# Kernel tuning notes

Hardware: AMD Instinct MI355X
Metric: run time of the kernel (lower is better)

Reference implementation:

```python
import jax, jax.numpy as jnp
import numpy as np


def _causal_kernel_mask(K):
    # casual_mask[i, K-i:] = 0 for i in 1..p
    p = K // 2
    m = np.ones((p + 1, K), np.float32)
    for i in range(1, p + 1):
        m[i, K - i:] = 0.0
    return jnp.asarray(m)


def setup_inputs() -> dict:
    rng = jax.random.key(0)
    k0, k1, k2, k3, k4 = jax.random.split(rng, 5)
    B, H, N, F = 2, 16, 1024, 64
    V, K = 32000, 5
    return {
        "input_ids": jax.random.randint(k0, (B, N), 0, V),
        "query": jax.random.normal(k1, (B, H, N, F), dtype=jnp.float32),
        "key": jax.random.normal(k2, (B, H, N, F), dtype=jnp.float32),
        "value": jax.random.normal(k3, (B, H, N, F), dtype=jnp.float32),
        "emb_weight": jax.random.normal(k4, (V, 2 * K), dtype=jnp.float32) * 0.02,
    }


def reference(input_ids, query, key, value, emb_weight):
    B, H, N, F = query.shape
    K = emb_weight.shape[1] // 2  # head/layer invariant -> emb dim = 2*K
    p = K // 2
    G = 2 * H

    # ---- get_kernel (layer 0; head_invariant + layer_invariant) ----
    kern = emb_weight[input_ids]                       # [B,N,2K]
    kern = kern.reshape(B, N, 2, 1, K)                 # [B,N,2,1,K]
    kern = jnp.broadcast_to(kern, (B, N, 2, H, K)).reshape(B, N, G, K)

    # ---- conv_key_value (for_casual=True, strict_on_casual=True) ----
    kv = jnp.concatenate([key, value], axis=1)         # [B,2H,N,F]
    kv_pad = jnp.pad(kv, ((0, 0), (0, 0), (p, p), (0, 0)))
    # unfold over token dim: [B,2H,K,N,F]
    kv_unf = jnp.stack([kv_pad[:, :, k:k + N, :] for k in range(K)], axis=2)
    cmask = _causal_kernel_mask(K)                     # [p+1,K]
    kern_m = kern[:, :, :, None, :] * cmask[None, None, None]  # [B,N,2H,p+1,K]
    # dynamic depthwise conv with per-offset causal masking
    out = jnp.einsum('bgknf,bngjk->bgjnf', kv_unf, kern_m)     # [B,2H,p+1,N,F]
    key_c = out[:, :H, 0]                              # [B,H,N,F]
    value_c = out[:, H:, 0]                            # [B,H,N,F]

    # ---- attention with causal-boundary corrections (n_past = 0) ----
    scale = 1.0 / jnp.sqrt(jnp.asarray(F, dtype=query.dtype))
    q = query * scale
    scores = jnp.einsum('bhnf,bhmf->bhnm', q, key_c)   # [B,H,N,N]

    # correct_attn_weights_near_casual_boundary
    for i in range(p):
        off = p - 1 - i
        cb_key = out[:, :H, 1 + i]                     # [B,H,N,F]
        corr = jnp.einsum('bhnf,bhnf->bhn', q[:, :, off:, :], cb_key[:, :, :N - off, :])
        rows = jnp.arange(N - off) + off
        cols = jnp.arange(N - off)
        scores = scores.at[:, :, rows, cols].set(corr)

    causal = jnp.tril(jnp.ones((N, N), dtype=bool))
    scores = jnp.where(causal, scores, jnp.asarray(-1e9, dtype=scores.dtype))
    probs = jax.nn.softmax(scores, axis=-1)
    attn = jnp.einsum('bhnm,bhmf->bhnf', probs, value_c)

    # correct_attn_output_near_casual_boundary
    for i in range(p):
        off = p - 1 - i
        cb_value = out[:, H:, 1 + i]                   # [B,H,N,F]
        idx = jnp.arange(N - off)
        diag_w = probs[:, :, idx + off, idx]           # diag offset=-off: [B,H,N-off]
        diff_v = cb_value[:, :, :N - off, :] - value_c[:, :, :N - off, :]
        diff = diag_w[..., None] * diff_v
        attn = attn + jnp.pad(diff, ((0, 0), (0, 0), (off, 0), (0, 0)))

    return attn
```

## Files before the change

### kernel.cpp

```cpp
#include <hip/hip_runtime.h>

#define HD    64
#define NSEQ  1024
#define NSLOT 40
#define LOG2E 1.44269504088896f

typedef __attribute__((ext_vector_type(8))) __bf16 bf16x8;
typedef __attribute__((ext_vector_type(4))) float  f32x4;
typedef __attribute__((ext_vector_type(4))) unsigned short u16x4;

__device__ __constant__ unsigned char PAIRS[NSLOT] = {
    60,61,62,63, 56,57,58, 52,53,54, 48,49,50, 44,45,46,
    40,41, 36,37, 32,33, 28,29, 24, 20, 16, 12,
    59, 42, 25, 8, 55, 38, 21, 4, 51, 34, 17, 0 };

__device__ inline unsigned short f2bf(float x) {
    unsigned u = __float_as_uint(x);
    return (unsigned short)((u + 0x7fffu + ((u >> 16) & 1u)) >> 16);
}
__device__ inline unsigned pk2(float a, float b) {
    return (unsigned)f2bf(a) | ((unsigned)f2bf(b) << 16);
}
__device__ inline float dot4(f32x4 a, f32x4 b) {
    return a.x * b.x + a.y * b.y + a.z * b.z + a.w * b.w;
}

__global__ __launch_bounds__(256) void conv_kernel(
    const int* __restrict__ ids,
    const float* __restrict__ keyg,
    const float* __restrict__ valg,
    const float* __restrict__ qg,
    const float* __restrict__ emb,
    unsigned short* __restrict__ kc,
    unsigned short* __restrict__ vcT,
    float* __restrict__ dg1, float* __restrict__ dg2)
{
    __shared__ __align__(16) float sA[70 * 68];
    __shared__ __align__(16) float sB[70 * 68];
    __shared__ float sE[65 * 10];

    int pid = blockIdx.x;
    int bh = pid & 31;
    int n0 = (pid >> 5) << 6;
    int b  = bh >> 4;
    int t  = threadIdx.x;
    size_t hb = (size_t)bh * NSEQ * HD;
    const float* kb = keyg + hb;
    const float* vb = valg + hb;

    for (int u = t; u < 650; u += 256) {
        int r = u / 10, c = u - r * 10;
        int n = n0 - 1 + r;
        sE[u] = (n >= 0) ? emb[(size_t)ids[b * NSEQ + n] * 10 + c] : 0.f;
    }
    for (int u = t; u < 70 * 16; u += 256) {
        int r = u >> 4, f = (u & 15) << 2;
        int g = n0 - 3 + r;
        f32x4 kv4 = (f32x4){0.f, 0.f, 0.f, 0.f};
        f32x4 vv4 = (f32x4){0.f, 0.f, 0.f, 0.f};
        if (g >= 0 && g < NSEQ) {
            kv4 = *(const f32x4*)(kb + (size_t)g * HD + f);
            vv4 = *(const f32x4*)(vb + (size_t)g * HD + f);
        }
        *(f32x4*)(sA + r * 68 + f) = kv4;
        *(f32x4*)(sB + r * 68 + f) = vv4;
    }
    __syncthreads();

    f32x4 vcv_save[4];
#pragma unroll
    for (int i = 0; i < 4; ++i) {
        int u  = (i << 8) + t;
        int nl = u >> 4, g4 = u & 15;
        int n  = n0 + nl, f = g4 << 2;
        const float* e  = sE + (nl + 1) * 10;
        const float* ep = sE + nl * 10;
        const float* ar = sA + nl * 68 + f;
        const float* br = sB + nl * 68 + f;
        f32x4 km3 = *(const f32x4*)(ar);
        f32x4 x0 = *(const f32x4*)(ar + 68);
        f32x4 x1 = *(const f32x4*)(ar + 2 * 68);
        f32x4 x2 = *(const f32x4*)(ar + 3 * 68);
        f32x4 x3 = *(const f32x4*)(ar + 4 * 68);
        f32x4 x4 = *(const f32x4*)(ar + 5 * 68);
        f32x4 v0 = *(const f32x4*)(br + 68);
        f32x4 v1 = *(const f32x4*)(br + 2 * 68);
        f32x4 v2 = *(const f32x4*)(br + 3 * 68);
        f32x4 v3 = *(const f32x4*)(br + 4 * 68);
        f32x4 v4 = *(const f32x4*)(br + 5 * 68);
        f32x4 qv = *(const f32x4*)(qg + hb + (size_t)n * HD + f) * (0.125f * LOG2E);

        f32x4 k012 = e[0] * x0 + e[1] * x1 + e[2] * x2;
        f32x4 kcv  = k012 + e[3] * x3 + e[4] * x4;
        f32x4 vcv  = e[5] * v0 + e[6] * v1 + e[7] * v2 + e[8] * v3 + e[9] * v4;

        u16x4 kq;
        kq.x = f2bf(kcv.x); kq.y = f2bf(kcv.y); kq.z = f2bf(kcv.z); kq.w = f2bf(kcv.w);
        *(u16x4*)(kc + hb + (size_t)n * HD + f) = kq;
        vcv_save[i] = vcv;

        float s2 = dot4(qv, k012);
        f32x4 kj1 = ep[0] * km3 + ep[1] * x0 + ep[2] * x1 + ep[3] * x2;
        float s1 = dot4(qv, kj1);
#pragma unroll
        for (int o = 1; o < 16; o <<= 1) {
            s2 += __shfl_xor(s2, o, 64);
            s1 += __shfl_xor(s1, o, 64);
        }
        if (g4 == 0) {
            dg2[bh * NSEQ + n] = s2;
            dg1[bh * NSEQ + n] = s1;
        }
    }
    __syncthreads();
    float* vt = sA;
#pragma unroll
    for (int i = 0; i < 4; ++i) {
        int u = (i << 8) + t;
        int nl = u >> 4, f = (u & 15) << 2;
        *(f32x4*)(vt + nl * 68 + f) = vcv_save[i];
    }
    __syncthreads();
#pragma unroll
    for (int i = 0; i < 4; ++i) {
        int u = (i << 8) + t;
        int f = u >> 4, nn = (u & 15) << 2;
        u16x4 o;
        o.x = f2bf(vt[(nn + 0) * 68 + f]);
        o.y = f2bf(vt[(nn + 1) * 68 + f]);
        o.z = f2bf(vt[(nn + 2) * 68 + f]);
        o.w = f2bf(vt[(nn + 3) * 68 + f]);
        *(u16x4*)(vcT + ((size_t)bh * HD + f) * NSEQ + n0 + nn) = o;
    }
}

__global__ __launch_bounds__(256, 4) void attn_kernel(
    const float* __restrict__ qg,
    const unsigned short* __restrict__ kc,
    const unsigned short* __restrict__ vcT,
    const float* __restrict__ dg1, const float* __restrict__ dg2,
    const float* __restrict__ valg, const int* __restrict__ ids,
    const float* __restrict__ emb,
    float* __restrict__ pML, unsigned short* __restrict__ pO,
    float* __restrict__ outg)
{
    __shared__ __align__(16) unsigned char sK[2][8192];
    __shared__ __align__(16) unsigned char sV[2][8192];
    __shared__ __align__(16) unsigned char sP[8192];

    int pid  = blockIdx.x;
    int bh   = pid & 31;
    int slot = pid >> 5;
    int code = PAIRS[slot];
    int j = code >> 2, cch = code & 3;
    int q0 = j << 6;
    int t0 = cch << 2;
    int len = j - (cch << 2) + 1; if (len > 4) len = 4;
    int nc  = (j >> 2) + 1;

    int t = threadIdx.x;
    int w = t >> 6, l = t & 63;
    int lq = l & 15, h = l >> 4, l7 = l & 7;
    int lid = h * 16 + lq;
    int qbw = q0 + w * 16;
    size_t hb = (size_t)bh * NSEQ * HD;

    const unsigned short* kcb = kc  + hb;
    const unsigned short* vtb = vcT + (size_t)bh * HD * NSEQ;

    bf16x8 qb0, qb1;
    {
        const float* qr = qg + hb + (size_t)(qbw + lq) * HD + 8 * h;
        f32x4 a0 = *(const f32x4*)(qr);
        f32x4 a1 = *(const f32x4*)(qr + 4);
        f32x4 b0 = *(const f32x4*)(qr + 32);
        f32x4 b1 = *(const f32x4*)(qr + 36);
        const float S = 0.125f * LOG2E;
        union { unsigned u[4]; bf16x8 v; } u0, u1;
        u0.u[0] = pk2(a0.x * S, a0.y * S); u0.u[1] = pk2(a0.z * S, a0.w * S);
        u0.u[2] = pk2(a1.x * S, a1.y * S); u0.u[3] = pk2(a1.z * S, a1.w * S);
        u1.u[0] = pk2(b0.x * S, b0.y * S); u1.u[1] = pk2(b0.z * S, b0.w * S);
        u1.u[2] = pk2(b1.x * S, b1.y * S); u1.u[3] = pk2(b1.z * S, b1.w * S);
        qb0 = u0.v; qb1 = u1.v;
    }
    float diag2_l = dg2[bh * NSEQ + qbw + lq];
    float diag1_l = dg1[bh * NSEQ + qbw + lq];

    f32x4 of[4];
#pragma unroll
    for (int ft = 0; ft < 4; ++ft) of[ft] = (f32x4){0.f, 0.f, 0.f, 0.f};
    float denom = 0.f;

    const int ka_off0 = ((0 + h) ^ l7) << 4;
    const int ka_off1 = ((4 + h) ^ l7) << 4;
    const int pr_base = w * 2048 + lq * 128;
    const int chk0 = ((qbw > 0 ? qbw - 1 : 0) >> 6);

    uint4 pf[4];
    auto issue = [&](int tg) {
        int kv0 = tg << 6;
#pragma unroll
        for (int i = 0; i < 4; ++i) {
            int chunk = t + (i << 8);
            int buf = chunk >> 9, loc = chunk & 511;
            int r = loc >> 3, c = loc & 7;
            int cs = c ^ (r & 7);
            pf[i] = (buf == 0)
                ? *(const uint4*)(kcb + (size_t)(kv0 + r) * HD + cs * 8)
                : *(const uint4*)(vtb + (size_t)r * NSEQ + kv0 + cs * 8);
        }
    };
    auto commit = [&](int cu) {
#pragma unroll
        for (int i = 0; i < 4; ++i) {
            int chunk = t + (i << 8);
            int buf = chunk >> 9, loc = chunk & 511;
            int r = loc >> 3, c = loc & 7;
            *(uint4*)((buf ? sV[cu] : sK[cu]) + r * 128 + c * 16) = pf[i];
        }
    };

    issue(t0); commit(0);
    if (len > 1) issue(t0 + 1);
    __syncthreads();

    for (int ti = 0; ti < len; ++ti) {
        int cur = ti & 1;
        if (ti + 1 < len) commit(cur ^ 1);
        if (ti + 2 < len) issue(t0 + ti + 2);
        int tg  = t0 + ti;
        int kv0 = tg << 6;
        const unsigned char* sKc = sK[cur];
        const unsigned char* sVc = sV[cur];

        f32x4 p[4];
        __builtin_amdgcn_s_setprio(1);
#pragma unroll
        for (int st = 0; st < 4; ++st) {
            bf16x8 ka0 = *(const bf16x8*)(sKc + st * 2048 + lq * 128 + ka_off0);
            bf16x8 ka1 = *(const bf16x8*)(sKc + st * 2048 + lq * 128 + ka_off1);
            f32x4 d = (f32x4){0.f, 0.f, 0.f, 0.f};
            d = __builtin_amdgcn_mfma_f32_16x16x32_bf16(ka0, qb0, d, 0, 0, 0);
            d = __builtin_amdgcn_mfma_f32_16x16x32_bf16(ka1, qb1, d, 0, 0, 0);
            p[st] = d;
        }
        __builtin_amdgcn_s_setprio(0);

        if (tg >= chk0) {
            int n_l = qbw + lq;
#pragma unroll
            for (int st = 0; st < 4; ++st)
#pragma unroll
                for (int r = 0; r < 4; ++r) {
                    int kv = kv0 + st * 16 + 4 * h + r;
                    float dd = p[st][r];
                    if (kv > n_l)           dd = -1e30f;
                    else if (kv == n_l)     dd = diag2_l;
                    else if (kv == n_l - 1) dd = diag1_l;
                    p[st][r] = dd;
                }
        }

        float lsum = 0.f;
#pragma unroll
        for (int st = 0; st < 4; ++st)
#pragma unroll
            for (int r = 0; r < 4; ++r) {
                float e = __builtin_exp2f(p[st][r]);
                p[st][r] = e;
                lsum += e;
            }
        lsum += __shfl_xor(lsum, 16, 64);
        lsum += __shfl_xor(lsum, 32, 64);
        denom += lsum;

#pragma unroll
        for (int st = 0; st < 4; ++st) {
            uint2 uu;
            uu.x = pk2(p[st][0], p[st][1]);
            uu.y = pk2(p[st][2], p[st][3]);
            int chunk = (st << 1) + (h >> 1);
            *(uint2*)(sP + pr_base + ((chunk ^ l7) << 4) + ((h & 1) << 3)) = uu;
        }
        asm volatile("s_waitcnt lgkmcnt(0)" ::: "memory");
        __builtin_amdgcn_sched_barrier(0);

        __builtin_amdgcn_s_setprio(1);
#pragma unroll
        for (int kk = 0; kk < 2; ++kk) {
            int koff = kk ? ka_off1 : ka_off0;
            bf16x8 pa = *(const bf16x8*)(sP + pr_base + koff);
#pragma unroll
            for (int ft = 0; ft < 4; ++ft) {
                bf16x8 vb = *(const bf16x8*)(sVc + ft * 2048 + lq * 128 + koff);
                of[ft] = __builtin_amdgcn_mfma_f32_16x16x32_bf16(pa, vb, of[ft], 0, 0, 0);
            }
        }
        __builtin_amdgcn_s_setprio(0);
        if (ti + 1 < len) __syncthreads();
    }

    int psBase = ((bh << 4) | j) << 2;
    if (nc > 1) {
        if (h == 0) {
            float2 ml; ml.x = 0.f; ml.y = denom;
            *(float2*)(pML + ((size_t)(psBase + cch) * 64 + w * 16 + lq) * 2) = ml;
        }
#pragma unroll
        for (int ft = 0; ft < 4; ++ft)
#pragma unroll
            for (int r = 0; r < 4; ++r)
                pO[(size_t)((((psBase + cch) * 4 + w) * 4 + ft) * 4 + r) * 64 + lid] =
                    f2bf(of[ft][r]);
        return;
    }

    const float* vraw = valg + hb;
    float* outr = outg + hb;
    const int* idb = ids + (size_t)(bh >> 4) * NSEQ;
#pragma unroll
    for (int r = 0; r < 4; ++r) {
        int qrow = 4 * h + r;
        int n = qbw + qrow;
        float dn = __shfl(denom,   qrow, 64);
        float d2 = __shfl(diag2_l, qrow, 64);
        float d1 = __shfl(diag1_l, qrow, 64);
        float inv = 1.0f / dn;
        float p2 = __builtin_exp2f(d2) * inv;
        float p1 = (n >= 1) ? __builtin_exp2f(d1) * inv : 0.f;
        int id_n = idb[n];
        float e8  = emb[(size_t)id_n * 10 + 8];
        float e9  = emb[(size_t)id_n * 10 + 9];
        float e9p = (n >= 1) ? emb[(size_t)idb[n - 1] * 10 + 9] : 0.f;
        float ca = -(p2 * e8 + p1 * e9p);
        float cb = -p2 * e9;
#pragma unroll
        for (int ft = 0; ft < 4; ++ft) {
            int f = ft * 16 + lq;
            float v = of[ft][r] * inv;
            if (n + 1 < NSEQ) v += ca * vraw[(size_t)(n + 1) * HD + f];
            if (n + 2 < NSEQ) v += cb * vraw[(size_t)(n + 2) * HD + f];
            outr[(size_t)n * HD + f] = v;
        }
    }
}

__global__ __launch_bounds__(256) void merge_kernel(
    const float* __restrict__ pML, const unsigned short* __restrict__ pO,
    const float* __restrict__ dg1, const float* __restrict__ dg2,
    const float* __restrict__ valg, const int* __restrict__ ids,
    const float* __restrict__ emb, float* __restrict__ outg)
{
    int pid = blockIdx.x;
    int bh = pid & 31, j = (pid >> 5) + 4;
    int nc = (j >> 2) + 1;
    int t = threadIdx.x;
    int rloc = t >> 2, fg = t & 3;
    int n = (j << 6) + rloc;
    int f0 = fg << 4;
    size_t hb = (size_t)bh * NSEQ * HD;
    int psBase = ((bh << 4) | j) << 2;

    float mc[4], lc[4];
    float mg = -3e30f;
    for (int c = 0; c < nc; ++c) {
        float2 v = *(const float2*)(pML + ((size_t)(psBase + c) * 64 + rloc) * 2);
        mc[c] = v.x; lc[c] = v.y;
        mg = fmaxf(mg, mc[c]);
    }
    float D = 0.f;
    f32x4 a0 = (f32x4){0.f,0.f,0.f,0.f}, a1 = a0, a2 = a0, a3 = a0;
    for (int c = 0; c < nc; ++c) {
        float wc = __builtin_exp2f(mc[c] - mg);
        D += lc[c] * wc;
        const unsigned short* pp = pO +
            (size_t)((((psBase + c) * 4 + (rloc >> 4)) * 4 + fg) * 4 + (rloc & 3)) * 64
            + ((rloc >> 2) & 3) * 16;
        uint4 ua = *(const uint4*)(pp);
        uint4 ub = *(const uint4*)(pp + 8);
        a0.x += wc * __uint_as_float(ua.x << 16);
        a0.y += wc * __uint_as_float(ua.x & 0xffff0000u);
        a0.z += wc * __uint_as_float(ua.y << 16);
        a0.w += wc * __uint_as_float(ua.y & 0xffff0000u);
        a1.x += wc * __uint_as_float(ua.z << 16);
        a1.y += wc * __uint_as_float(ua.z & 0xffff0000u);
        a1.z += wc * __uint_as_float(ua.w << 16);
        a1.w += wc * __uint_as_float(ua.w & 0xffff0000u);
        a2.x += wc * __uint_as_float(ub.x << 16);
        a2.y += wc * __uint_as_float(ub.x & 0xffff0000u);
        a2.z += wc * __uint_as_float(ub.y << 16);
        a2.w += wc * __uint_as_float(ub.y & 0xffff0000u);
        a3.x += wc * __uint_as_float(ub.z << 16);
        a3.y += wc * __uint_as_float(ub.z & 0xffff0000u);
        a3.z += wc * __uint_as_float(ub.w << 16);
        a3.w += wc * __uint_as_float(ub.w & 0xffff0000u);
    }
    float inv = 1.0f / D;
    float d2 = dg2[bh * NSEQ + n], d1 = dg1[bh * NSEQ + n];
    float p2 = __builtin_exp2f(d2 - mg) * inv;
    float p1 = __builtin_exp2f(d1 - mg) * inv;
    const int* idb = ids + (size_t)(bh >> 4) * NSEQ;
    int id_n = idb[n];
    float e8  = emb[(size_t)id_n * 10 + 8];
    float e9  = emb[(size_t)id_n * 10 + 9];
    float e9p = emb[(size_t)idb[n - 1] * 10 + 9];
    float ca = -(p2 * e8 + p1 * e9p);
    float cb = -p2 * e9;

    a0 *= inv; a1 *= inv; a2 *= inv; a3 *= inv;
    if (n + 1 < NSEQ) {
        const float* v1 = valg + hb + (size_t)(n + 1) * HD + f0;
        a0 += ca * *(const f32x4*)(v1);
        a1 += ca * *(const f32x4*)(v1 + 4);
        a2 += ca * *(const f32x4*)(v1 + 8);
        a3 += ca * *(const f32x4*)(v1 + 12);
    }
    if (n + 2 < NSEQ) {
        const float* v2 = valg + hb + (size_t)(n + 2) * HD + f0;
        a0 += cb * *(const f32x4*)(v2);
        a1 += cb * *(const f32x4*)(v2 + 4);
        a2 += cb * *(const f32x4*)(v2 + 8);
        a3 += cb * *(const f32x4*)(v2 + 12);
    }
    float* o = outg + hb + (size_t)n * HD + f0;
    *(f32x4*)(o)      = a0;
    *(f32x4*)(o + 4)  = a1;
    *(f32x4*)(o + 8)  = a2;
    *(f32x4*)(o + 12) = a3;
}

extern "C" void kernel_launch(void* const* d_in, const int* in_sizes, int n_in,
                              void* d_out, int out_size, void* d_ws, size_t ws_size,
                              hipStream_t stream)
{
    const int*   ids = (const int*)  d_in[0];
    const float* q   = (const float*)d_in[1];
    const float* key = (const float*)d_in[2];
    const float* val = (const float*)d_in[3];
    const float* emb = (const float*)d_in[4];
    float* out = (float*)d_out;

    char* w = (char*)d_ws;
    unsigned short* kc  = (unsigned short*)(w);
    unsigned short* vcT = (unsigned short*)(w + (4u << 20));
    float* dg1 = (float*)(w + 8388608);
    float* dg2 = (float*)(w + 8519680);
    float* pML = (float*)(w + 8650752);
    unsigned short* pO = (unsigned short*)(w + 9699328);

    conv_kernel<<<512, 256, 0, stream>>>(ids, key, val, q, emb, kc, vcT, dg1, dg2);
    attn_kernel<<<32 * NSLOT, 256, 0, stream>>>(q, kc, vcT, dg1, dg2, val, ids, emb,
                                                pML, pO, out);
    merge_kernel<<<384, 256, 0, stream>>>(pML, pO, dg1, dg2, val, ids, emb, out);
}
```

Baseline: 56.16 us.

## Split KV range across two wave groups in-block and drop merge kernel

```diff
diff --git a/kernel.cpp b/kernel.cpp
--- a/kernel.cpp
+++ b/kernel.cpp
@@ -2,17 +2,11 @@
 
 #define HD    64
 #define NSEQ  1024
-#define NSLOT 40
 #define LOG2E 1.44269504088896f
 
 typedef __attribute__((ext_vector_type(8))) __bf16 bf16x8;
 typedef __attribute__((ext_vector_type(4))) float  f32x4;
 typedef __attribute__((ext_vector_type(4))) unsigned short u16x4;
-
-__device__ __constant__ unsigned char PAIRS[NSLOT] = {
-    60,61,62,63, 56,57,58, 52,53,54, 48,49,50, 44,45,46,
-    40,41, 36,37, 32,33, 28,29, 24, 20, 16, 12,
-    59, 42, 25, 8, 55, 38, 21, 4, 51, 34, 17, 0 };
 
 __device__ inline unsigned short f2bf(float x) {
     unsigned u = __float_as_uint(x);
@@ -134,35 +128,32 @@
     }
 }
 
-__global__ __launch_bounds__(256, 4) void attn_kernel(
+__global__ __launch_bounds__(512, 4) void attn_kernel(
     const float* __restrict__ qg,
     const unsigned short* __restrict__ kc,
     const unsigned short* __restrict__ vcT,
     const float* __restrict__ dg1, const float* __restrict__ dg2,
     const float* __restrict__ valg, const int* __restrict__ ids,
     const float* __restrict__ emb,
-    float* __restrict__ pML, unsigned short* __restrict__ pO,
     float* __restrict__ outg)
 {
-    __shared__ __align__(16) unsigned char sK[2][8192];
-    __shared__ __align__(16) unsigned char sV[2][8192];
-    __shared__ __align__(16) unsigned char sP[8192];
-
-    int pid  = blockIdx.x;
-    int bh   = pid & 31;
-    int slot = pid >> 5;
-    int code = PAIRS[slot];
-    int j = code >> 2, cch = code & 3;
-    int q0 = j << 6;
-    int t0 = cch << 2;
-    int len = j - (cch << 2) + 1; if (len > 4) len = 4;
-    int nc  = (j >> 2) + 1;
-
-    int t = threadIdx.x;
-    int w = t >> 6, l = t & 63;
+    __shared__ __align__(16) unsigned char sK[2][2][8192];
+    __shared__ __align__(16) unsigned char sV[2][2][8192];
+    __shared__ __align__(16) unsigned char sP[16384];
+
+    int pid = blockIdx.x;
+    int bh  = pid & 31;
+    int j   = 15 - (pid >> 5);
+    int t   = threadIdx.x;
+    int wv  = t >> 6, l = t & 63;
+    int grp = wv >> 2;
+    int w_in = wv & 3;
     int lq = l & 15, h = l >> 4, l7 = l & 7;
-    int lid = h * 16 + lq;
-    int qbw = q0 + w * 16;
+    int qbw = j * 64 + w_in * 16;
+    int hA  = (j + 2) >> 1;
+    int t0  = grp ? hA : 0;
+    int myLen = grp ? (j + 1 - hA) : hA;
+    int L   = hA;
     size_t hb = (size_t)bh * NSEQ * HD;
 
     const unsigned short* kcb = kc  + hb;
@@ -193,15 +184,16 @@
 
     const int ka_off0 = ((0 + h) ^ l7) << 4;
     const int ka_off1 = ((4 + h) ^ l7) << 4;
-    const int pr_base = w * 2048 + lq * 128;
+    const int pr_base = wv * 2048 + lq * 128;
     const int chk0 = ((qbw > 0 ? qbw - 1 : 0) >> 6);
 
+    const int tl = t & 255;
     uint4 pf[4];
     auto issue = [&](int tg) {
         int kv0 = tg << 6;
 #pragma unroll
         for (int i = 0; i < 4; ++i) {
-            int chunk = t + (i << 8);
+            int chunk = tl + (i << 8);
             int buf = chunk >> 9, loc = chunk & 511;
             int r = loc >> 3, c = loc & 7;
             int cs = c ^ (r & 7);
@@ -213,106 +205,122 @@
     auto commit = [&](int cu) {
 #pragma unroll
         for (int i = 0; i < 4; ++i) {
-            int chunk = t + (i << 8);
+            int chunk = tl + (i << 8);
             int buf = chunk >> 9, loc = chunk & 511;
             int r = loc >> 3, c = loc & 7;
-            *(uint4*)((buf ? sV[cu] : sK[cu]) + r * 128 + c * 16) = pf[i];
+            *(uint4*)((buf ? sV[grp][cu] : sK[grp][cu]) + r * 128 + c * 16) = pf[i];
         }
     };
 
-    issue(t0); commit(0);
-    if (len > 1) issue(t0 + 1);
-    __syncthreads();
-
-    for (int ti = 0; ti < len; ++ti) {
+    if (myLen > 0) { issue(t0); commit(0); }
+    if (myLen > 1) issue(t0 + 1);
+    __syncthreads();
+
+    for (int ti = 0; ti < L; ++ti) {
         int cur = ti & 1;
-        if (ti + 1 < len) commit(cur ^ 1);
-        if (ti + 2 < len) issue(t0 + ti + 2);
+        if (ti + 1 < myLen) commit(cur ^ 1);
+        if (ti + 2 < myLen) issue(t0 + ti + 2);
         int tg  = t0 + ti;
         int kv0 = tg << 6;
-        const unsigned char* sKc = sK[cur];
-        const unsigned char* sVc = sV[cur];
-
-        f32x4 p[4];
-        __builtin_amdgcn_s_setprio(1);
-#pragma unroll
-        for (int st = 0; st < 4; ++st) {
-            bf16x8 ka0 = *(const bf16x8*)(sKc + st * 2048 + lq * 128 + ka_off0);
-            bf16x8 ka1 = *(const bf16x8*)(sKc + st * 2048 + lq * 128 + ka_off1);
-            f32x4 d = (f32x4){0.f, 0.f, 0.f, 0.f};
-            d = __builtin_amdgcn_mfma_f32_16x16x32_bf16(ka0, qb0, d, 0, 0, 0);
-            d = __builtin_amdgcn_mfma_f32_16x16x32_bf16(ka1, qb1, d, 0, 0, 0);
-            p[st] = d;
-        }
-        __builtin_amdgcn_s_setprio(0);
-
-        if (tg >= chk0) {
-            int n_l = qbw + lq;
+        bool act = (ti < myLen);
+
+        if (act) {
+            const unsigned char* sKc = sK[grp][cur];
+            const unsigned char* sVc = sV[grp][cur];
+            f32x4 p[4];
+            __builtin_amdgcn_s_setprio(1);
+#pragma unroll
+            for (int st = 0; st < 4; ++st) {
+                bf16x8 ka0 = *(const bf16x8*)(sKc + st * 2048 + lq * 128 + ka_off0);
+                bf16x8 ka1 = *(const bf16x8*)(sKc + st * 2048 + lq * 128 + ka_off1);
+                f32x4 d = (f32x4){0.f, 0.f, 0.f, 0.f};
+                d = __builtin_amdgcn_mfma_f32_16x16x32_bf16(ka0, qb0, d, 0, 0, 0);
+                d = __builtin_amdgcn_mfma_f32_16x16x32_bf16(ka1, qb1, d, 0, 0, 0);
+                p[st] = d;
+            }
+            __builtin_amdgcn_s_setprio(0);
+
+            if (tg >= chk0) {
+                int n_l = qbw + lq;
+#pragma unroll
+                for (int st = 0; st < 4; ++st)
+#pragma unroll
+                    for (int r = 0; r < 4; ++r) {
+                        int kv = kv0 + st * 16 + 4 * h + r;
+                        float dd = p[st][r];
+                        if (kv > n_l)           dd = -1e30f;
+                        else if (kv == n_l)     dd = diag2_l;
+                        else if (kv == n_l - 1) dd = diag1_l;
+                        p[st][r] = dd;
+                    }
+            }
+
+            float lsum = 0.f;
 #pragma unroll
             for (int st = 0; st < 4; ++st)
 #pragma unroll
                 for (int r = 0; r < 4; ++r) {
-                    int kv = kv0 + st * 16 + 4 * h + r;
-                    float dd = p[st][r];
-                    if (kv > n_l)           dd = -1e30f;
-                    else if (kv == n_l)     dd = diag2_l;
-                    else if (kv == n_l - 1) dd = diag1_l;
-                    p[st][r] = dd;
+                    float e = __builtin_exp2f(p[st][r]);
+                    p[st][r] = e;
+                    lsum += e;
                 }
-        }
-
-        float lsum = 0.f;
-#pragma unroll
-        for (int st = 0; st < 4; ++st)
-#pragma unroll
-            for (int r = 0; r < 4; ++r) {
-                float e = __builtin_exp2f(p[st][r]);
-                p[st][r] = e;
-                lsum += e;
+            lsum += __shfl_xor(lsum, 16, 64);
+            lsum += __shfl_xor(lsum, 32, 64);
+            denom += lsum;
+
+#pragma unroll
+            for (int st = 0; st < 4; ++st) {
+                uint2 uu;
+                uu.x = pk2(p[st][0], p[st][1]);
+                uu.y = pk2(p[st][2], p[st][3]);
+                int chunk = (st << 1) + (h >> 1);
+                *(uint2*)(sP + pr_base + ((chunk ^ l7) << 4) + ((h & 1) << 3)) = uu;
             }
-        lsum += __shfl_xor(lsum, 16, 64);
-        lsum += __shfl_xor(lsum, 32, 64);
-        denom += lsum;
-
-#pragma unroll
-        for (int st = 0; st < 4; ++st) {
-            uint2 uu;
-            uu.x = pk2(p[st][0], p[st][1]);
-            uu.y = pk2(p[st][2], p[st][3]);
-            int chunk = (st << 1) + (h >> 1);
-            *(uint2*)(sP + pr_base + ((chunk ^ l7) << 4) + ((h & 1) << 3)) = uu;
-        }
-        asm volatile("s_waitcnt lgkmcnt(0)" ::: "memory");
-        __builtin_amdgcn_sched_barrier(0);
-
-        __builtin_amdgcn_s_setprio(1);
-#pragma unroll
-        for (int kk = 0; kk < 2; ++kk) {
-            int koff = kk ? ka_off1 : ka_off0;
-            bf16x8 pa = *(const bf16x8*)(sP + pr_base + koff);
-#pragma unroll
-            for (int ft = 0; ft < 4; ++ft) {
-                bf16x8 vb = *(const bf16x8*)(sVc + ft * 2048 + lq * 128 + koff);
-                of[ft] = __builtin_amdgcn_mfma_f32_16x16x32_bf16(pa, vb, of[ft], 0, 0, 0);
+            asm volatile("s_waitcnt lgkmcnt(0)" ::: "memory");
+            __builtin_amdgcn_sched_barrier(0);
+
+            __builtin_amdgcn_s_setprio(1);
+#pragma unroll
+            for (int kk = 0; kk < 2; ++kk) {
+                int koff = kk ? ka_off1 : ka_off0;
+                bf16x8 pa = *(const bf16x8*)(sP + pr_base + koff);
+#pragma unroll
+                for (int ft = 0; ft < 4; ++ft) {
+                    bf16x8 vb = *(const bf16x8*)(sVc + ft * 2048 + lq * 128 + koff);
+                    of[ft] = __builtin_amdgcn_mfma_f32_16x16x32_bf16(pa, vb, of[ft], 0, 0, 0);
+                }
             }
-        }
-        __builtin_amdgcn_s_setprio(0);
-        if (ti + 1 < len) __syncthreads();
-    }
-
-    int psBase = ((bh << 4) | j) << 2;
-    if (nc > 1) {
-        if (h == 0) {
-            float2 ml; ml.x = 0.f; ml.y = denom;
-            *(float2*)(pML + ((size_t)(psBase + cch) * 64 + w * 16 + lq) * 2) = ml;
-        }
-#pragma unroll
-        for (int ft = 0; ft < 4; ++ft)
-#pragma unroll
-            for (int r = 0; r < 4; ++r)
-                pO[(size_t)((((psBase + cch) * 4 + w) * 4 + ft) * 4 + r) * 64 + lid] =
-                    f2bf(of[ft][r]);
-        return;
+            __builtin_amdgcn_s_setprio(0);
+        }
+        if (ti + 1 < L) __syncthreads();
+    }
+
+    __syncthreads();
+    float* mrg = (float*)sK;
+    if (grp == 1) {
+        float* d = mrg + (size_t)tl * 17;
+#pragma unroll
+        for (int ft = 0; ft < 4; ++ft) {
+            d[4 * ft + 0] = of[ft].x;
+            d[4 * ft + 1] = of[ft].y;
+            d[4 * ft + 2] = of[ft].z;
+            d[4 * ft + 3] = of[ft].w;
+        }
+        d[16] = denom;
+    }
+    __syncthreads();
+    if (grp == 1) return;
+
+    {
+        const float* s = mrg + (size_t)tl * 17;
+#pragma unroll
+        for (int ft = 0; ft < 4; ++ft) {
+            of[ft].x += s[4 * ft + 0];
+            of[ft].y += s[4 * ft + 1];
+            of[ft].z += s[4 * ft + 2];
+            of[ft].w += s[4 * ft + 3];
+        }
+        denom += s[16];
     }
 
     const float* vraw = valg + hb;
@@ -345,90 +353,6 @@
     }
 }
 
-__global__ __launch_bounds__(256) void merge_kernel(
-    const float* __restrict__ pML, const unsigned short* __restrict__ pO,
-    const float* __restrict__ dg1, const float* __restrict__ dg2,
-    const float* __restrict__ valg, const int* __restrict__ ids,
-    const float* __restrict__ emb, float* __restrict__ outg)
-{
-    int pid = blockIdx.x;
-    int bh = pid & 31, j = (pid >> 5) + 4;
-    int nc = (j >> 2) + 1;
-    int t = threadIdx.x;
-    int rloc = t >> 2, fg = t & 3;
-    int n = (j << 6) + rloc;
-    int f0 = fg << 4;
-    size_t hb = (size_t)bh * NSEQ * HD;
-    int psBase = ((bh << 4) | j) << 2;
-
-    float mc[4], lc[4];
-    float mg = -3e30f;
-    for (int c = 0; c < nc; ++c) {
-        float2 v = *(const float2*)(pML + ((size_t)(psBase + c) * 64 + rloc) * 2);
-        mc[c] = v.x; lc[c] = v.y;
-        mg = fmaxf(mg, mc[c]);
-    }
-    float D = 0.f;
-    f32x4 a0 = (f32x4){0.f,0.f,0.f,0.f}, a1 = a0, a2 = a0, a3 = a0;
-    for (int c = 0; c < nc; ++c) {
-        float wc = __builtin_exp2f(mc[c] - mg);
-        D += lc[c] * wc;
-        const unsigned short* pp = pO +
-            (size_t)((((psBase + c) * 4 + (rloc >> 4)) * 4 + fg) * 4 + (rloc & 3)) * 64
-            + ((rloc >> 2) & 3) * 16;
-        uint4 ua = *(const uint4*)(pp);
-        uint4 ub = *(const uint4*)(pp + 8);
-        a0.x += wc * __uint_as_float(ua.x << 16);
-        a0.y += wc * __uint_as_float(ua.x & 0xffff0000u);
-        a0.z += wc * __uint_as_float(ua.y << 16);
-        a0.w += wc * __uint_as_float(ua.y & 0xffff0000u);
-        a1.x += wc * __uint_as_float(ua.z << 16);
-        a1.y += wc * __uint_as_float(ua.z & 0xffff0000u);
-        a1.z += wc * __uint_as_float(ua.w << 16);
-        a1.w += wc * __uint_as_float(ua.w & 0xffff0000u);
-        a2.x += wc * __uint_as_float(ub.x << 16);
-        a2.y += wc * __uint_as_float(ub.x & 0xffff0000u);
-        a2.z += wc * __uint_as_float(ub.y << 16);
-        a2.w += wc * __uint_as_float(ub.y & 0xffff0000u);
-        a3.x += wc * __uint_as_float(ub.z << 16);
-        a3.y += wc * __uint_as_float(ub.z & 0xffff0000u);
-        a3.z += wc * __uint_as_float(ub.w << 16);
-        a3.w += wc * __uint_as_float(ub.w & 0xffff0000u);
-    }
-    float inv = 1.0f / D;
-    float d2 = dg2[bh * NSEQ + n], d1 = dg1[bh * NSEQ + n];
-    float p2 = __builtin_exp2f(d2 - mg) * inv;
-    float p1 = __builtin_exp2f(d1 - mg) * inv;
-    const int* idb = ids + (size_t)(bh >> 4) * NSEQ;
-    int id_n = idb[n];
-    float e8  = emb[(size_t)id_n * 10 + 8];
-    float e9  = emb[(size_t)id_n * 10 + 9];
-    float e9p = emb[(size_t)idb[n - 1] * 10 + 9];
-    float ca = -(p2 * e8 + p1 * e9p);
-    float cb = -p2 * e9;
-
-    a0 *= inv; a1 *= inv; a2 *= inv; a3 *= inv;
-    if (n + 1 < NSEQ) {
-        const float* v1 = valg + hb + (size_t)(n + 1) * HD + f0;
-        a0 += ca * *(const f32x4*)(v1);
-        a1 += ca * *(const f32x4*)(v1 + 4);
-        a2 += ca * *(const f32x4*)(v1 + 8);
-        a3 += ca * *(const f32x4*)(v1 + 12);
-    }
-    if (n + 2 < NSEQ) {
-        const float* v2 = valg + hb + (size_t)(n + 2) * HD + f0;
-        a0 += cb * *(const f32x4*)(v2);
-        a1 += cb * *(const f32x4*)(v2 + 4);
-        a2 += cb * *(const f32x4*)(v2 + 8);
-        a3 += cb * *(const f32x4*)(v2 + 12);
-    }
-    float* o = outg + hb + (size_t)n * HD + f0;
-    *(f32x4*)(o)      = a0;
-    *(f32x4*)(o + 4)  = a1;
-    *(f32x4*)(o + 8)  = a2;
-    *(f32x4*)(o + 12) = a3;
-}
-
 extern "C" void kernel_launch(void* const* d_in, const int* in_sizes, int n_in,
                               void* d_out, int out_size, void* d_ws, size_t ws_size,
                               hipStream_t stream)
@@ -445,11 +369,7 @@
     unsigned short* vcT = (unsigned short*)(w + (4u << 20));
     float* dg1 = (float*)(w + 8388608);
     float* dg2 = (float*)(w + 8519680);
-    float* pML = (float*)(w + 8650752);
-    unsigned short* pO = (unsigned short*)(w + 9699328);
 
     conv_kernel<<<512, 256, 0, stream>>>(ids, key, val, q, emb, kc, vcT, dg1, dg2);
-    attn_kernel<<<32 * NSLOT, 256, 0, stream>>>(q, kc, vcT, dg1, dg2, val, ids, emb,
-                                                pML, pO, out);
-    merge_kernel<<<384, 256, 0, stream>>>(pML, pO, dg1, dg2, val, ids, emb, out);
-}
+    attn_kernel<<<512, 512, 0, stream>>>(q, kc, vcT, dg1, dg2, val, ids, emb, out);
+}
```

New measurement: 54.37 us. 1.03x faster.
